# Kernel tuning notes

Hardware: AMD Instinct MI355X
Metric: run time of the kernel (lower is better)

The kernel has to match this reference:

```python
import jax, jax.numpy as jnp
import numpy as np

HEAD_DIM = 64
N_HEADS = 64
N_KV = 8
Q_MULT = N_HEADS // N_KV  # 8
HIDDEN = 2880
SEQ = 1024
BATCH = 2
SLIDING_WINDOW = 128  # layer_idx=0 -> window active
ROPE_THETA = 150000.0
SCALING = 32.0
NTK_ALPHA = 1.0
NTK_BETA = 32.0
INIT_CTX = 4096
EPS = 1e-5


def _rope_caches(seq_len):
    # YaRN rotary caches (static numpy precompute, as in the source module)
    steps = np.arange(0, HEAD_DIM, 2, dtype=np.float32)
    freq = np.power(np.float32(ROPE_THETA), steps / np.float32(HEAD_DIM))
    concentration = np.float32(0.1) * np.log(np.float32(SCALING)) + 1.0
    d_half = np.float32(HEAD_DIM / 2.0)
    log_base = np.log(np.float32(ROPE_THETA))
    low = d_half * np.log(np.float32(INIT_CTX) / (np.float32(NTK_BETA) * np.float32(2.0 * np.pi))) / log_base
    high = d_half * np.log(np.float32(INIT_CTX) / (np.float32(NTK_ALPHA) * np.float32(2.0 * np.pi))) / log_base
    ramp = (np.arange(HEAD_DIM // 2, dtype=np.float32) - low) / (high - low)
    mask = 1.0 - np.clip(ramp, 0.0, 1.0)
    inv_freq = (1.0 / (np.float32(SCALING) * freq)) * (1.0 - mask) + (1.0 / freq) * mask
    pos = np.arange(seq_len, dtype=np.float32)
    freqs = np.einsum('i,j->ij', pos, inv_freq.astype(np.float32))
    cos = (np.cos(freqs) * concentration).astype(np.float32)
    sin = (np.sin(freqs) * concentration).astype(np.float32)
    return jnp.asarray(cos), jnp.asarray(sin)


def _apply_rotary(t, cos, sin):
    # t: (B, S, ..., head_dim); cos/sin: (S, head_dim//2). Rotate-half style.
    shape = (1, t.shape[1]) + (1,) * (t.ndim - 3) + (cos.shape[-1],)
    c = cos.reshape(shape)
    s = sin.reshape(shape)
    first, second = jnp.split(t, 2, axis=-1)
    return jnp.concatenate([first * c - second * s, second * c + first * s], axis=-1)


def setup_inputs() -> dict:
    key = jax.random.key(0)
    ks = jax.random.split(key, 6)
    qkv_dim = (N_HEADS + 2 * N_KV) * HEAD_DIM  # 5120
    return {
        'x': jax.random.normal(ks[0], (BATCH, SEQ, HIDDEN), dtype=jnp.float32),
        'norm_w': jnp.ones((HIDDEN,), dtype=jnp.float32),
        'qkv_w': jax.random.normal(ks[1], (qkv_dim, HIDDEN), dtype=jnp.float32) * 0.02,
        'qkv_b': jax.random.normal(ks[2], (qkv_dim,), dtype=jnp.float32) * 0.02,
        'out_w': jax.random.normal(ks[3], (HIDDEN, N_HEADS * HEAD_DIM), dtype=jnp.float32) * 0.02,
        'out_b': jax.random.normal(ks[4], (HIDDEN,), dtype=jnp.float32) * 0.02,
        'sinks': jax.random.normal(ks[5], (N_HEADS,), dtype=jnp.float32),
    }


def reference(x, norm_w, qkv_w, qkv_b, out_w, out_b, sinks):
    B, S, _ = x.shape
    # RMSNorm (fp32 accumulation)
    xf = x.astype(jnp.float32)
    rms = jnp.mean(xf * xf, axis=-1, keepdims=True)
    t = (xf * jax.lax.rsqrt(rms + EPS) * norm_w).astype(x.dtype)
    # QKV projection (fp32 accumulation)
    qkv = jnp.matmul(t.astype(jnp.float32), qkv_w.T) + qkv_b
    q_dim = N_HEADS * HEAD_DIM
    kv_dim = N_KV * HEAD_DIM
    q = qkv[..., :q_dim].reshape(B, S, N_KV, Q_MULT, HEAD_DIM)
    k = qkv[..., q_dim:q_dim + kv_dim].reshape(B, S, N_KV, HEAD_DIM)
    v = qkv[..., q_dim + kv_dim:].reshape(B, S, N_KV, HEAD_DIM)
    # YaRN rotary embedding
    cos, sin = _rope_caches(S)
    q = _apply_rotary(q, cos, sin)
    k = _apply_rotary(k, cos, sin)
    # causal + sliding-window mask
    neg_inf = jnp.float32(-jnp.inf)
    mask = jnp.triu(jnp.full((S, S), neg_inf, dtype=jnp.float32), k=1)
    mask = mask + jnp.tril(jnp.full((S, S), neg_inf, dtype=jnp.float32), k=-SLIDING_WINDOW)
    sm_scale = jnp.float32(1.0 / np.sqrt(HEAD_DIM))
    # GQA attention with sink logits
    logits = jnp.einsum('bqhmd,bkhd->bhmqk', q, k) * sm_scale + mask[None, None, None]
    sink = jnp.broadcast_to(sinks.reshape(1, N_KV, Q_MULT, 1, 1), (B, N_KV, Q_MULT, S, 1))
    logits = jnp.concatenate([logits, sink], axis=-1)
    w = jax.nn.softmax(logits, axis=-1)[..., :-1]  # drop sink column
    attn = jnp.einsum('bhmqk,bkhd->bqhmd', w, v).reshape(B, S, N_HEADS * HEAD_DIM)
    # output projection (fp32 accumulation) + residual
    out = jnp.matmul(attn, out_w.T) + out_b
    return x + out
```

## Files before the change

### kernel.cpp

```cpp
#include <hip/hip_runtime.h>

typedef unsigned short ushort_t;
typedef __attribute__((ext_vector_type(8))) short short8;
typedef __attribute__((ext_vector_type(8))) __bf16 bf16x8;
typedef __attribute__((ext_vector_type(4))) float float4v;
typedef __attribute__((ext_vector_type(4))) unsigned int uint4v;

__device__ __forceinline__ float bf2f(ushort_t u) {
    unsigned int v = ((unsigned int)u) << 16;
    return __builtin_bit_cast(float, v);
}
__device__ __forceinline__ ushort_t f2bf(float f) {
    unsigned int u = __builtin_bit_cast(unsigned int, f);
    unsigned int lsb = (u >> 16) & 1u;
    u += 0x7fffu + lsb;
    return (ushort_t)(u >> 16);
}
__device__ __forceinline__ uint4v pack8(const ushort_t* r) {
    uint4v u;
#pragma unroll
    for (int i = 0; i < 4; ++i)
        u[i] = (unsigned int)r[2 * i] | ((unsigned int)r[2 * i + 1] << 16);
    return u;
}
__device__ __forceinline__ void unpack8(uint4v u, float* f) {
#pragma unroll
    for (int i = 0; i < 4; ++i) {
        unsigned int x = u[i];
        f[2 * i] = __builtin_bit_cast(float, x << 16);
        f[2 * i + 1] = __builtin_bit_cast(float, x & 0xffff0000u);
    }
}
__device__ __forceinline__ uint4v ld8f32_bf(const float* p) {
    float4v a = *(const float4v*)p;
    float4v b = *(const float4v*)(p + 4);
    ushort_t r[8];
#pragma unroll
    for (int j = 0; j < 4; ++j) { r[j] = f2bf(a[j]); r[4 + j] = f2bf(b[j]); }
    return pack8(r);
}

template <typename V>
__device__ __forceinline__ auto mfma_sel(V a, V b, float4v c, int)
    -> decltype(__builtin_amdgcn_mfma_f32_16x16x32_bf16(a, b, c, 0, 0, 0)) {
    return __builtin_amdgcn_mfma_f32_16x16x32_bf16(a, b, c, 0, 0, 0);
}
template <typename V>
__device__ __forceinline__ float4v mfma_sel(V a, V b, float4v c, long) {
    return __builtin_amdgcn_mfma_f32_16x16x32_bf16(__builtin_bit_cast(bf16x8, a),
                                                   __builtin_bit_cast(bf16x8, b), c, 0, 0, 0);
}
__device__ __forceinline__ float4v mfma_bf16(short8 a, short8 b, float4v c) {
    return mfma_sel(a, b, c, 0);
}

__device__ __forceinline__ float wave_sum(float v) {
#pragma unroll
    for (int o = 32; o; o >>= 1) v += __shfl_xor(v, o);
    return v;
}

#define HIDDEN 2880
#define NTOK 2048
#define QKV_DIM 5120
#define ATTN_DIM 4096
#define SM_SCALE 0.125f

__global__ __launch_bounds__(256) void f32_to_bf16_kernel(const float* __restrict__ in,
                                                          ushort_t* __restrict__ out, int n8) {
    int idx = blockIdx.x * 256 + threadIdx.x;
    if (idx < n8) *(uint4v*)(out + (size_t)idx * 8) = ld8f32_bf(in + (size_t)idx * 8);
}

__global__ __launch_bounds__(256) void rmsnorm_kernel(const float* __restrict__ x,
                                                      const float* __restrict__ wgt,
                                                      ushort_t* __restrict__ out) {
    const int tok = blockIdx.x, tid = threadIdx.x;
    const float* xr = x + (size_t)tok * HIDDEN;
    float v[16];
    float ss = 0.f;
#pragma unroll
    for (int i = 0; i < 2; ++i) {
        int c = tid + i * 256;
        if (c < 360) {
            float4v a = *(const float4v*)(xr + c * 8);
            float4v b = *(const float4v*)(xr + c * 8 + 4);
#pragma unroll
            for (int j = 0; j < 4; ++j) { v[i * 8 + j] = a[j]; v[i * 8 + 4 + j] = b[j]; }
#pragma unroll
            for (int j = 0; j < 8; ++j) ss += v[i * 8 + j] * v[i * 8 + j];
        }
    }
    ss = wave_sum(ss);
    __shared__ float red[4];
    if ((tid & 63) == 0) red[tid >> 6] = ss;
    __syncthreads();
    float scale = rsqrtf((red[0] + red[1] + red[2] + red[3]) * (1.f / 2880.f) + 1e-5f);
#pragma unroll
    for (int i = 0; i < 2; ++i) {
        int c = tid + i * 256;
        if (c < 360) {
            float4v wa = *(const float4v*)(wgt + c * 8);
            float4v wb = *(const float4v*)(wgt + c * 8 + 4);
            ushort_t r[8];
#pragma unroll
            for (int j = 0; j < 4; ++j) {
                r[j] = f2bf(v[i * 8 + j] * scale * wa[j]);
                r[4 + j] = f2bf(v[i * 8 + 4 + j] * scale * wb[j]);
            }
            *(uint4v*)(out + (size_t)tok * HIDDEN + c * 8) = pack8(r);
        }
    }
}

__global__ __launch_bounds__(256) void rope_apply_kernel(ushort_t* __restrict__ qkv) {
    int idx = blockIdx.x * 256 + threadIdx.x;
    int tok = idx / 288;
    int rem = idx - tok * 288;
    int h = rem >> 2, dg = rem & 3;
    int s = tok & 1023;
    size_t base = (size_t)tok * QKV_DIM + (h < 64 ? h * 64 : 4096 + (h - 64) * 64) + dg * 8;
    uint4v u1 = *(const uint4v*)(qkv + base);
    uint4v u2 = *(const uint4v*)(qkv + base + 32);
    float f1[8], f2[8];
    unpack8(u1, f1);
    unpack8(u2, f2);
    const float step = (float)(11.918390573078392 / 32.0);
    const float conc = (float)(1.3465735902799727);
    const float low = (float)(8.092890725542669);
    const float invden = (float)(1.0 / 9.305804387286162);
    ushort_t r1[8], r2[8];
#pragma unroll
    for (int jj = 0; jj < 8; ++jj) {
        int j = dg * 8 + jj;
        float invf = __expf(-(float)j * step);
        float ramp = ((float)j - low) * invden;
        float mask = 1.f - fminf(fmaxf(ramp, 0.f), 1.f);
        float inv_freq = invf * ((1.f - mask) * 0.03125f + mask);
        float ang = (float)s * inv_freq;
        float c = cosf(ang) * conc;
        float sn = sinf(ang) * conc;
        r1[jj] = f2bf(f1[jj] * c - f2[jj] * sn);
        r2[jj] = f2bf(f2[jj] * c + f1[jj] * sn);
    }
    *(uint4v*)(qkv + base) = pack8(r1);
    *(uint4v*)(qkv + base + 32) = pack8(r2);
}

template <int BN, bool RESID, bool OUTF32, bool BF16B>
__global__ __launch_bounds__(256) void gemm_kernel(const ushort_t* __restrict__ A,
                                                   const void* __restrict__ B,
                                                   const float* __restrict__ bias,
                                                   const float* __restrict__ resid,
                                                   void* __restrict__ Cout, int M, int N, int K) {
    constexpr int BM = 128, BK = 64;
    constexpr int LDT = BK + 8;
    static_assert(BN == 128 || BN == 64, "");
    __shared__ __align__(16) ushort_t As[BM * LDT];
    __shared__ __align__(16) ushort_t Bs[BN * LDT];

    const int m0 = blockIdx.x * BM;
    const int n0 = blockIdx.y * BN;
    const int tid = threadIdx.x;
    const int w = tid >> 6, lane = tid & 63;
    const int quad = lane >> 4, l16 = lane & 15;

    constexpr int WN = BN / 2;
    constexpr int NI = WN / 16;
    const int wm = (w >> 1) * 64;
    const int wn = (w & 1) * WN;

    constexpr int ACH = BM * BK / 8 / 256;
    constexpr int BCH = BN * BK / 8 / 256;

    float4v acc[4][NI];
#pragma unroll
    for (int i = 0; i < 4; ++i)
#pragma unroll
        for (int j = 0; j < NI; ++j) acc[i][j] = (float4v){0.f, 0.f, 0.f, 0.f};

    const int nk = K / BK;
    uint4v areg[ACH], breg[BCH];

#pragma unroll
    for (int i = 0; i < ACH; ++i) {
        int c = tid + i * 256, r = c >> 3, col = c & 7;
        areg[i] = *(const uint4v*)(A + (size_t)(m0 + r) * K + col * 8);
    }
#pragma unroll
    for (int i = 0; i < BCH; ++i) {
        int c = tid + i * 256, r = c >> 3, col = c & 7;
        if constexpr (BF16B) breg[i] = *(const uint4v*)((const ushort_t*)B + (size_t)(n0 + r) * K + col * 8);
        else breg[i] = ld8f32_bf((const float*)B + (size_t)(n0 + r) * K + col * 8);
    }

    for (int kt = 0; kt < nk; ++kt) {
        __syncthreads();
#pragma unroll
        for (int i = 0; i < ACH; ++i) {
            int c = tid + i * 256, r = c >> 3, col = c & 7;
            *(uint4v*)(As + r * LDT + col * 8) = areg[i];
        }
#pragma unroll
        for (int i = 0; i < BCH; ++i) {
            int c = tid + i * 256, r = c >> 3, col = c & 7;
            *(uint4v*)(Bs + r * LDT + col * 8) = breg[i];
        }
        __syncthreads();
        if (kt + 1 < nk) {
            const int k0 = (kt + 1) * BK;
#pragma unroll
            for (int i = 0; i < ACH; ++i) {
                int c = tid + i * 256, r = c >> 3, col = c & 7;
                areg[i] = *(const uint4v*)(A + (size_t)(m0 + r) * K + k0 + col * 8);
            }
#pragma unroll
            for (int i = 0; i < BCH; ++i) {
                int c = tid + i * 256, r = c >> 3, col = c & 7;
                if constexpr (BF16B) breg[i] = *(const uint4v*)((const ushort_t*)B + (size_t)(n0 + r) * K + k0 + col * 8);
                else breg[i] = ld8f32_bf((const float*)B + (size_t)(n0 + r) * K + k0 + col * 8);
            }
        }
#pragma unroll
        for (int ks = 0; ks < 2; ++ks) {
            short8 af[4], bfr[NI];
#pragma unroll
            for (int mi = 0; mi < 4; ++mi)
                af[mi] = *(const short8*)(As + (wm + mi * 16 + l16) * LDT + ks * 32 + quad * 8);
#pragma unroll
            for (int ni = 0; ni < NI; ++ni)
                bfr[ni] = *(const short8*)(Bs + (wn + ni * 16 + l16) * LDT + ks * 32 + quad * 8);
#pragma unroll
            for (int mi = 0; mi < 4; ++mi)
#pragma unroll
                for (int ni = 0; ni < NI; ++ni)
                    acc[mi][ni] = mfma_bf16(af[mi], bfr[ni], acc[mi][ni]);
        }
    }

#pragma unroll
    for (int ni = 0; ni < NI; ++ni) {
        int gc = n0 + wn + ni * 16 + l16;
        float bv = bias[gc];
#pragma unroll
        for (int mi = 0; mi < 4; ++mi) {
#pragma unroll
            for (int r = 0; r < 4; ++r) {
                int gr = m0 + wm + mi * 16 + quad * 4 + r;
                float vv = acc[mi][ni][r] + bv;
                if constexpr (RESID) vv += resid[(size_t)gr * N + gc];
                if constexpr (OUTF32) ((float*)Cout)[(size_t)gr * N + gc] = vv;
                else ((ushort_t*)Cout)[(size_t)gr * N + gc] = f2bf(vv);
            }
        }
    }
}

__global__ __launch_bounds__(256, 1) void attn_mfma_kernel(const ushort_t* __restrict__ qkv,
                                                           const float* __restrict__ sinks,
                                                           ushort_t* __restrict__ attnbuf) {
    constexpr int LDK = 72, LDV = 200, LDP = 200;
    __shared__ __align__(16) ushort_t Ks[192 * LDK];
    __shared__ __align__(16) ushort_t Vt[64 * LDV];
    __shared__ __align__(16) ushort_t Pb[4][16 * LDP];

    const int qc = blockIdx.x, kvh = blockIdx.y, b = blockIdx.z;
    const int tid = threadIdx.x;
    const int w = tid >> 6, lane = tid & 63;
    const int quad = lane >> 4, l16 = lane & 15;
    const int w0 = qc * 64 - 127;

    for (int c = tid; c < 192 * 8; c += 256) {
        int row = c >> 3, col8 = c & 7;
        int pos = w0 + row;
        pos = pos < 0 ? 0 : (pos > 1023 ? 1023 : pos);
        size_t gk = ((size_t)(b * 1024 + pos)) * QKV_DIM + 4096 + kvh * 64 + col8 * 8;
        *(uint4v*)(Ks + row * LDK + col8 * 8) = *(const uint4v*)(qkv + gk);
        uint4v vv = *(const uint4v*)(qkv + gk + 512);
        ushort_t vs[8];
#pragma unroll
        for (int i = 0; i < 4; ++i) {
            vs[2 * i] = (ushort_t)(vv[i] & 0xffffu);
            vs[2 * i + 1] = (ushort_t)(vv[i] >> 16);
        }
#pragma unroll
        for (int j = 0; j < 8; ++j) Vt[(col8 * 8 + j) * LDV + row] = vs[j];
    }
    __syncthreads();

    short8 Vf[6][4];
#pragma unroll
    for (int kt = 0; kt < 6; ++kt)
#pragma unroll
        for (int nv = 0; nv < 4; ++nv)
            Vf[kt][nv] = *(const short8*)(Vt + (nv * 16 + l16) * LDV + kt * 32 + quad * 8);

    ushort_t* Pw = Pb[w];

    for (int mt = 0; mt < 8; ++mt) {
        const int h = kvh * 8 + w * 2 + (mt >> 2);
        const int qtile = mt & 3;
        const int tokb = b * 1024 + qc * 64 + qtile * 16;
        const float sink_f = sinks[h];

        short8 qf[2];
        {
            const ushort_t* qp = qkv + ((size_t)(tokb + l16)) * QKV_DIM + h * 64 + quad * 8;
            qf[0] = *(const short8*)qp;
            qf[1] = *(const short8*)(qp + 32);
        }

        float4v acc[12];
#pragma unroll
        for (int nt = 0; nt < 12; ++nt) acc[nt] = (float4v){0.f, 0.f, 0.f, 0.f};
#pragma unroll
        for (int nt = 0; nt < 12; ++nt) {
#pragma unroll
            for (int ks = 0; ks < 2; ++ks) {
                short8 kf = *(const short8*)(Ks + (nt * 16 + l16) * LDK + ks * 32 + quad * 8);
                acc[nt] = mfma_bf16(qf[ks], kf, acc[nt]);
            }
        }

        float linv[4];
#pragma unroll
        for (int r = 0; r < 4; ++r) {
            const int ql = qtile * 16 + quad * 4 + r;
            float e[12];
            float mx = -1e30f;
#pragma unroll
            for (int nt = 0; nt < 12; ++nt) {
                int row_k = nt * 16 + l16;
                bool valid = (row_k >= ql) && (row_k <= ql + 127) && (w0 + row_k >= 0);
                float s = valid ? acc[nt][r] * SM_SCALE : -1e30f;
                e[nt] = s;
                mx = fmaxf(mx, s);
            }
#pragma unroll
            for (int o = 1; o < 16; o <<= 1) mx = fmaxf(mx, __shfl_xor(mx, o));
            float M = fmaxf(mx, sink_f);
            float ls = 0.f;
#pragma unroll
            for (int nt = 0; nt < 12; ++nt) {
                float ev = (e[nt] > -1e29f) ? __expf(e[nt] - M) : 0.f;
                e[nt] = ev;
                ls += ev;
            }
#pragma unroll
            for (int o = 1; o < 16; o <<= 1) ls += __shfl_xor(ls, o);
            linv[r] = 1.f / (ls + __expf(sink_f - M));
#pragma unroll
            for (int nt = 0; nt < 12; ++nt)
                Pw[(quad * 4 + r) * LDP + nt * 16 + l16] = f2bf(e[nt]);
        }

        float4v accO[4];
#pragma unroll
        for (int nv = 0; nv < 4; ++nv) accO[nv] = (float4v){0.f, 0.f, 0.f, 0.f};
#pragma unroll
        for (int kt = 0; kt < 6; ++kt) {
            short8 pf = *(const short8*)(Pw + l16 * LDP + kt * 32 + quad * 8);
#pragma unroll
            for (int nv = 0; nv < 4; ++nv) accO[nv] = mfma_bf16(pf, Vf[kt][nv], accO[nv]);
        }

#pragma unroll
        for (int r = 0; r < 4; ++r) {
            size_t ob = ((size_t)(tokb + quad * 4 + r)) * ATTN_DIM + h * 64 + l16;
#pragma unroll
            for (int nv = 0; nv < 4; ++nv)
                attnbuf[ob + nv * 16] = f2bf(accO[nv][r] * linv[r]);
        }
    }
}

extern "C" void kernel_launch(void* const* d_in, const int* in_sizes, int n_in,
                              void* d_out, int out_size, void* d_ws, size_t ws_size,
                              hipStream_t stream) {
    const float* x = (const float*)d_in[0];
    const float* norm_w = (const float*)d_in[1];
    const float* qkv_w = (const float*)d_in[2];
    const float* qkv_b = (const float*)d_in[3];
    const float* out_w = (const float*)d_in[4];
    const float* out_b = (const float*)d_in[5];
    const float* sinks = (const float*)d_in[6];
    float* outp = (float*)d_out;
    char* ws = (char*)d_ws;

    if (ws_size >= 86000000ull) {
        ushort_t* qkvbuf = (ushort_t*)ws;
        ushort_t* qkv_w_bf = (ushort_t*)(ws + 20971520);
        ushort_t* attnbuf = (ushort_t*)(ws + 20971520);
        ushort_t* Tbuf = (ushort_t*)(ws + 50462720);
        ushort_t* out_w_bf = (ushort_t*)(ws + 62259200);

        f32_to_bf16_kernel<<<7200, 256, 0, stream>>>(qkv_w, qkv_w_bf, 1843200);
        f32_to_bf16_kernel<<<5760, 256, 0, stream>>>(out_w, out_w_bf, 1474560);
        rmsnorm_kernel<<<NTOK, 256, 0, stream>>>(x, norm_w, Tbuf);
        gemm_kernel<128, false, false, true><<<dim3(16, 40), 256, 0, stream>>>(
            Tbuf, qkv_w_bf, qkv_b, nullptr, qkvbuf, NTOK, QKV_DIM, HIDDEN);
        rope_apply_kernel<<<2304, 256, 0, stream>>>(qkvbuf);
        attn_mfma_kernel<<<dim3(16, 8, 2), 256, 0, stream>>>(qkvbuf, sinks, attnbuf);
        gemm_kernel<64, true, true, true><<<dim3(16, 45), 256, 0, stream>>>(
            attnbuf, out_w_bf, out_b, x, outp, NTOK, HIDDEN, ATTN_DIM);
    } else {
        ushort_t* qkvbuf = (ushort_t*)ws;
        ushort_t* attnbuf = (ushort_t*)(ws + 20971520);
        ushort_t* Tbuf = (ushort_t*)d_out;

        rmsnorm_kernel<<<NTOK, 256, 0, stream>>>(x, norm_w, Tbuf);
        gemm_kernel<128, false, false, false><<<dim3(16, 40), 256, 0, stream>>>(
            Tbuf, qkv_w, qkv_b, nullptr, qkvbuf, NTOK, QKV_DIM, HIDDEN);
        rope_apply_kernel<<<2304, 256, 0, stream>>>(qkvbuf);
        attn_mfma_kernel<<<dim3(16, 8, 2), 256, 0, stream>>>(qkvbuf, sinks, attnbuf);
        gemm_kernel<64, true, true, false><<<dim3(16, 45), 256, 0, stream>>>(
            attnbuf, out_w, out_b, x, outp, NTOK, HIDDEN, ATTN_DIM);
    }
}
```

Measured before the change: 369.5 us.

## Use direct global-to-LDS loads with XOR swizzle, split attention heads, widen out-proj tile

On the bf16-weight path, the GEMM now stages A and B tiles with global_load_lds in place of register prefetch, and uses an XOR-swizzled unpadded LDS layout to avoid bank conflicts. This gives up the register double-buffer, so loads are no longer overlapped with compute inside a block. The attention grid is doubled so each block handles 4 heads instead of 8, with launch bounds raised to allow two blocks per CU. The output projection switches from BN=64 to BN=96 tiles.

```diff
diff --git a/kernel.cpp b/kernel.cpp
--- a/kernel.cpp
+++ b/kernel.cpp
@@ -39,6 +39,16 @@
     for (int j = 0; j < 4; ++j) { r[j] = f2bf(a[j]); r[4 + j] = f2bf(b[j]); }
     return pack8(r);
 }
+
+#if __has_builtin(__builtin_amdgcn_global_load_lds)
+#define HAVE_GLDS 1
+__device__ __forceinline__ void glds16(const ushort_t* gp, ushort_t* lp) {
+    __builtin_amdgcn_global_load_lds((const __attribute__((address_space(1))) void*)gp,
+                                     (__attribute__((address_space(3))) void*)lp, 16, 0, 0);
+}
+#else
+#define HAVE_GLDS 0
+#endif
 
 template <typename V>
 __device__ __forceinline__ auto mfma_sel(V a, V b, float4v c, int)
@@ -154,8 +164,8 @@
                                                    const float* __restrict__ resid,
                                                    void* __restrict__ Cout, int M, int N, int K) {
     constexpr int BM = 128, BK = 64;
-    constexpr int LDT = BK + 8;
-    static_assert(BN == 128 || BN == 64, "");
+    constexpr int LDT = BF16B ? 64 : 72;
+    static_assert(BN == 128 || BN == 96 || BN == 64, "");
     __shared__ __align__(16) ushort_t As[BM * LDT];
     __shared__ __align__(16) ushort_t Bs[BN * LDT];
 
@@ -170,66 +180,86 @@
     const int wm = (w >> 1) * 64;
     const int wn = (w & 1) * WN;
 
+    float4v acc[4][NI];
+#pragma unroll
+    for (int i = 0; i < 4; ++i)
+#pragma unroll
+        for (int j = 0; j < NI; ++j) acc[i][j] = (float4v){0.f, 0.f, 0.f, 0.f};
+
+    const int nk = K / BK;
+
+#if HAVE_GLDS
+    constexpr int NAI = BM / 32;
+    constexpr int NBI = BN / 32;
+#endif
     constexpr int ACH = BM * BK / 8 / 256;
     constexpr int BCH = BN * BK / 8 / 256;
 
-    float4v acc[4][NI];
-#pragma unroll
-    for (int i = 0; i < 4; ++i)
-#pragma unroll
-        for (int j = 0; j < NI; ++j) acc[i][j] = (float4v){0.f, 0.f, 0.f, 0.f};
-
-    const int nk = K / BK;
-    uint4v areg[ACH], breg[BCH];
-
-#pragma unroll
-    for (int i = 0; i < ACH; ++i) {
-        int c = tid + i * 256, r = c >> 3, col = c & 7;
-        areg[i] = *(const uint4v*)(A + (size_t)(m0 + r) * K + col * 8);
-    }
-#pragma unroll
-    for (int i = 0; i < BCH; ++i) {
-        int c = tid + i * 256, r = c >> 3, col = c & 7;
-        if constexpr (BF16B) breg[i] = *(const uint4v*)((const ushort_t*)B + (size_t)(n0 + r) * K + col * 8);
-        else breg[i] = ld8f32_bf((const float*)B + (size_t)(n0 + r) * K + col * 8);
-    }
-
     for (int kt = 0; kt < nk; ++kt) {
+        const int k0 = kt * BK;
         __syncthreads();
-#pragma unroll
-        for (int i = 0; i < ACH; ++i) {
-            int c = tid + i * 256, r = c >> 3, col = c & 7;
-            *(uint4v*)(As + r * LDT + col * 8) = areg[i];
-        }
-#pragma unroll
-        for (int i = 0; i < BCH; ++i) {
-            int c = tid + i * 256, r = c >> 3, col = c & 7;
-            *(uint4v*)(Bs + r * LDT + col * 8) = breg[i];
-        }
-        __syncthreads();
-        if (kt + 1 < nk) {
-            const int k0 = (kt + 1) * BK;
+        if constexpr (BF16B) {
+#if HAVE_GLDS
+            const ushort_t* Bp = (const ushort_t*)B;
+#pragma unroll
+            for (int i = 0; i < NAI; ++i) {
+                int sb = (w * NAI + i) * 64;
+                int s = sb + lane;
+                int r = s >> 3, p = s & 7, c = p ^ (r & 7);
+                glds16(A + (size_t)(m0 + r) * K + k0 + c * 8, As + sb * 8);
+            }
+#pragma unroll
+            for (int i = 0; i < NBI; ++i) {
+                int sb = (w * NBI + i) * 64;
+                int s = sb + lane;
+                int r = s >> 3, p = s & 7, c = p ^ (r & 7);
+                glds16(Bp + (size_t)(n0 + r) * K + k0 + c * 8, Bs + sb * 8);
+            }
+#else
 #pragma unroll
             for (int i = 0; i < ACH; ++i) {
                 int c = tid + i * 256, r = c >> 3, col = c & 7;
-                areg[i] = *(const uint4v*)(A + (size_t)(m0 + r) * K + k0 + col * 8);
+                *(uint4v*)(As + r * LDT + col * 8) =
+                    *(const uint4v*)(A + (size_t)(m0 + r) * K + k0 + col * 8);
             }
 #pragma unroll
             for (int i = 0; i < BCH; ++i) {
                 int c = tid + i * 256, r = c >> 3, col = c & 7;
-                if constexpr (BF16B) breg[i] = *(const uint4v*)((const ushort_t*)B + (size_t)(n0 + r) * K + k0 + col * 8);
-                else breg[i] = ld8f32_bf((const float*)B + (size_t)(n0 + r) * K + k0 + col * 8);
-            }
-        }
+                *(uint4v*)(Bs + r * LDT + col * 8) =
+                    *(const uint4v*)((const ushort_t*)B + (size_t)(n0 + r) * K + k0 + col * 8);
+            }
+#endif
+        } else {
+#pragma unroll
+            for (int i = 0; i < ACH; ++i) {
+                int c = tid + i * 256, r = c >> 3, col = c & 7;
+                *(uint4v*)(As + r * LDT + col * 8) =
+                    *(const uint4v*)(A + (size_t)(m0 + r) * K + k0 + col * 8);
+            }
+#pragma unroll
+            for (int i = 0; i < BCH; ++i) {
+                int c = tid + i * 256, r = c >> 3, col = c & 7;
+                *(uint4v*)(Bs + r * LDT + col * 8) =
+                    ld8f32_bf((const float*)B + (size_t)(n0 + r) * K + k0 + col * 8);
+            }
+        }
+        __syncthreads();
+
 #pragma unroll
         for (int ks = 0; ks < 2; ++ks) {
             short8 af[4], bfr[NI];
 #pragma unroll
-            for (int mi = 0; mi < 4; ++mi)
-                af[mi] = *(const short8*)(As + (wm + mi * 16 + l16) * LDT + ks * 32 + quad * 8);
-#pragma unroll
-            for (int ni = 0; ni < NI; ++ni)
-                bfr[ni] = *(const short8*)(Bs + (wn + ni * 16 + l16) * LDT + ks * 32 + quad * 8);
+            for (int mi = 0; mi < 4; ++mi) {
+                int row = wm + mi * 16 + l16;
+                int off = BF16B ? ((ks * 4 + quad) ^ (row & 7)) * 8 : ks * 32 + quad * 8;
+                af[mi] = *(const short8*)(As + row * LDT + off);
+            }
+#pragma unroll
+            for (int ni = 0; ni < NI; ++ni) {
+                int row = wn + ni * 16 + l16;
+                int off = BF16B ? ((ks * 4 + quad) ^ (row & 7)) * 8 : ks * 32 + quad * 8;
+                bfr[ni] = *(const short8*)(Bs + row * LDT + off);
+            }
 #pragma unroll
             for (int mi = 0; mi < 4; ++mi)
 #pragma unroll
@@ -256,7 +286,7 @@
     }
 }
 
-__global__ __launch_bounds__(256, 1) void attn_mfma_kernel(const ushort_t* __restrict__ qkv,
+__global__ __launch_bounds__(256, 2) void attn_mfma_kernel(const ushort_t* __restrict__ qkv,
                                                            const float* __restrict__ sinks,
                                                            ushort_t* __restrict__ attnbuf) {
     constexpr int LDK = 72, LDV = 200, LDP = 200;
@@ -264,7 +294,7 @@
     __shared__ __align__(16) ushort_t Vt[64 * LDV];
     __shared__ __align__(16) ushort_t Pb[4][16 * LDP];
 
-    const int qc = blockIdx.x, kvh = blockIdx.y, b = blockIdx.z;
+    const int qc = blockIdx.x, kvh = blockIdx.y >> 1, half = blockIdx.y & 1, b = blockIdx.z;
     const int tid = threadIdx.x;
     const int w = tid >> 6, lane = tid & 63;
     const int quad = lane >> 4, l16 = lane & 15;
@@ -296,12 +326,11 @@
             Vf[kt][nv] = *(const short8*)(Vt + (nv * 16 + l16) * LDV + kt * 32 + quad * 8);
 
     ushort_t* Pw = Pb[w];
-
-    for (int mt = 0; mt < 8; ++mt) {
-        const int h = kvh * 8 + w * 2 + (mt >> 2);
-        const int qtile = mt & 3;
+    const int h = kvh * 8 + half * 4 + w;
+    const float sink_f = sinks[h];
+
+    for (int qtile = 0; qtile < 4; ++qtile) {
         const int tokb = b * 1024 + qc * 64 + qtile * 16;
-        const float sink_f = sinks[h];
 
         short8 qf[2];
         {
@@ -400,8 +429,8 @@
         gemm_kernel<128, false, false, true><<<dim3(16, 40), 256, 0, stream>>>(
             Tbuf, qkv_w_bf, qkv_b, nullptr, qkvbuf, NTOK, QKV_DIM, HIDDEN);
         rope_apply_kernel<<<2304, 256, 0, stream>>>(qkvbuf);
-        attn_mfma_kernel<<<dim3(16, 8, 2), 256, 0, stream>>>(qkvbuf, sinks, attnbuf);
-        gemm_kernel<64, true, true, true><<<dim3(16, 45), 256, 0, stream>>>(
+        attn_mfma_kernel<<<dim3(16, 16, 2), 256, 0, stream>>>(qkvbuf, sinks, attnbuf);
+        gemm_kernel<96, true, true, true><<<dim3(16, 30), 256, 0, stream>>>(
             attnbuf, out_w_bf, out_b, x, outp, NTOK, HIDDEN, ATTN_DIM);
     } else {
         ushort_t* qkvbuf = (ushort_t*)ws;
@@ -412,8 +441,8 @@
         gemm_kernel<128, false, false, false><<<dim3(16, 40), 256, 0, stream>>>(
             Tbuf, qkv_w, qkv_b, nullptr, qkvbuf, NTOK, QKV_DIM, HIDDEN);
         rope_apply_kernel<<<2304, 256, 0, stream>>>(qkvbuf);
-        attn_mfma_kernel<<<dim3(16, 8, 2), 256, 0, stream>>>(qkvbuf, sinks, attnbuf);
-        gemm_kernel<64, true, true, false><<<dim3(16, 45), 256, 0, stream>>>(
+        attn_mfma_kernel<<<dim3(16, 16, 2), 256, 0, stream>>>(qkvbuf, sinks, attnbuf);
+        gemm_kernel<96, true, true, false><<<dim3(16, 30), 256, 0, stream>>>(
             attnbuf, out_w, out_b, x, outp, NTOK, HIDDEN, ATTN_DIM);
     }
 }
```

After: 391.6 us. 6.0% more time.
